# Optimization experiments

Measured on AMD Instinct MI355X. Metric: run time of the kernel, lower is better.

Reference implementation:

```python
import jax, jax.numpy as jnp
import numpy as np

B, N, DIN, DE, NH, DK = 4, 256, 128, 64, 8, 16


def setup_inputs() -> dict:
    key = jax.random.key(0)
    ks = jax.random.split(key, 8)
    s = 0.05
    return {
        "h": jax.random.normal(ks[0], (B, N, DIN), jnp.float32),
        "e": jax.random.normal(ks[1], (B, N, N, DE), jnp.float32),
        "mask": jnp.ones((B, N), jnp.float32),
        "WQ": jax.random.normal(ks[2], (DIN, NH * DK), jnp.float32) * s,
        "WK": jax.random.normal(ks[3], (DIN, NH * DK), jnp.float32) * s,
        "WV": jax.random.normal(ks[4], (DIN, NH * DK), jnp.float32) * s,
        "WE": jax.random.normal(ks[5], (DE, NH * DK), jnp.float32) * s,
        "WE2": jax.random.normal(ks[6], (DE, NH * DK), jnp.float32) * s,
    }


def reference(h, e, mask, WQ, WK, WV, WE, WE2):
    b, n, _ = h.shape
    Q = (h @ WQ).reshape(b, n, NH, DK)
    K = (h @ WK).reshape(b, n, NH, DK) * (float(DK) ** -0.5)
    V = (h @ WV).reshape(b, n, NH, DK)
    E = (e @ WE).reshape(b, n, n, NH, DK)
    E2 = (e @ WE2).reshape(b, n, n, NH, DK)
    # edge-augmented scores: (b, i, j, h, k)
    scores = jnp.einsum('bihk,bjhk->bijh', Q, K)[..., None] + E2
    scores = jnp.exp(jnp.clip(scores, -5.0, 5.0))
    attn_mask = mask[:, :, None, None, None] * mask[:, None, :, None, None]
    scores = scores * attn_mask
    softmax_denom = jnp.clip(scores.sum(axis=2), 1e-6, None)  # (b,i,h,k)
    scores = scores * attn_mask  # attn_dropout p=0.0 -> identity
    out = jnp.einsum('bijhk,bjhk->bihk', scores, V)
    out = out + (scores * E).sum(axis=2)
    out = out / softmax_denom
    return out.reshape(b, n, NH * DK)
```

## Files before the change

### kernel.cpp

```cpp
#include <hip/hip_runtime.h>

#define BB   4
#define NN   256
#define DIN  128
#define DE   64
#define NH   8
#define DK   16
#define CC   128

typedef __attribute__((ext_vector_type(8))) short short8;
typedef __attribute__((ext_vector_type(4))) float f32x4;

__device__ __forceinline__ unsigned short f2bfu(float f) {
    union { float f; unsigned int i; } v; v.f = f;
    unsigned int x = v.i;
    x += 0x7FFFu + ((x >> 16) & 1u);
    return (unsigned short)(x >> 16);
}

__global__ __launch_bounds__(256) void qkv_kernel(
    const float* __restrict__ h, const float* __restrict__ WQ,
    const float* __restrict__ WK, const float* __restrict__ WV,
    const float* __restrict__ WE, const float* __restrict__ WE2,
    float* __restrict__ Qw, float* __restrict__ Kw, float* __restrict__ Vt,
    unsigned short* __restrict__ wfrag)
{
    const int t = threadIdx.x;

    if (blockIdx.x >= 256) {
        const int tid  = (blockIdx.x - 256) * 256 + t;
        const int m    = tid >> 10;
        const int g    = (tid >> 7) & 7;
        const int ks   = (tid >> 6) & 1;
        const int lane = tid & 63;
        const int q4 = lane >> 4, l15 = lane & 15;
        const float* W = m ? WE2 : WE;
        union { uint4 u; unsigned short s[8]; } pk;
        #pragma unroll
        for (int ii = 0; ii < 8; ++ii) {
            const int d = ks * 32 + q4 * 8 + ii;
            pk.s[ii] = f2bfu(W[d * CC + g * 16 + l15]);
        }
        ((uint4*)wfrag)[tid] = pk.u;
        return;
    }

    __shared__ float hsh[4 * DIN];
    __shared__ float psum[4 * 1536];
    const int r0 = blockIdx.x * 4;

    hsh[t]       = h[(size_t)r0 * DIN + t];
    hsh[256 + t] = h[(size_t)r0 * DIN + 256 + t];
    __syncthreads();

    const int cp  = t & 63;
    const int qtr = t >> 6;
    float aq[4][2], ak[4][2], av[4][2];
    #pragma unroll
    for (int r = 0; r < 4; ++r)
        aq[r][0]=aq[r][1]=ak[r][0]=ak[r][1]=av[r][0]=av[r][1]=0.f;

    #pragma unroll 4
    for (int dd = 0; dd < 32; ++dd) {
        const int d = qtr * 32 + dd;
        const float2 fq = ((const float2*)WQ)[d * 64 + cp];
        const float2 fk = ((const float2*)WK)[d * 64 + cp];
        const float2 fv = ((const float2*)WV)[d * 64 + cp];
        #pragma unroll
        for (int r = 0; r < 4; ++r) {
            const float hd = hsh[r * DIN + d];
            aq[r][0] = fmaf(hd, fq.x, aq[r][0]); aq[r][1] = fmaf(hd, fq.y, aq[r][1]);
            ak[r][0] = fmaf(hd, fk.x, ak[r][0]); ak[r][1] = fmaf(hd, fk.y, ak[r][1]);
            av[r][0] = fmaf(hd, fv.x, av[r][0]); av[r][1] = fmaf(hd, fv.y, av[r][1]);
        }
    }
    float* pq = psum + qtr * 1536;
    #pragma unroll
    for (int r = 0; r < 4; ++r) {
        pq[r*384       + 2*cp] = aq[r][0]; pq[r*384       + 2*cp+1] = aq[r][1];
        pq[r*384 + 128 + 2*cp] = ak[r][0]; pq[r*384 + 128 + 2*cp+1] = ak[r][1];
        pq[r*384 + 256 + 2*cp] = av[r][0]; pq[r*384 + 256 + 2*cp+1] = av[r][1];
    }
    __syncthreads();

    const int b  = r0 >> 8;
    const int j0 = r0 & 255;
    #pragma unroll
    for (int k = 0; k < 6; ++k) {
        const int o = k * 256 + t;
        float v = psum[o] + psum[1536 + o] + psum[3072 + o] + psum[4608 + o];
        const int r   = o / 384;
        const int mc  = o - r * 384;
        const int mat = mc >> 7;
        const int c   = mc & 127;
        if      (mat == 0) Qw[(size_t)(r0 + r) * CC + c] = v;
        else if (mat == 1) Kw[(size_t)(r0 + r) * CC + c] = v * 0.25f;
        else               Vt[((size_t)(b * CC) + c) * NN + j0 + r] = v;
    }
}

__global__ __launch_bounds__(256) void attn_kernel(
    const float* __restrict__ e, const float* __restrict__ maskp,
    const unsigned short* __restrict__ wfrag,
    const float* __restrict__ Qw, const float* __restrict__ Kw,
    const float* __restrict__ Vt, float* __restrict__ out)
{
    __shared__ __align__(16) unsigned short esh[128 * DE];
    __shared__ __align__(16) float qk_sh[NH * NN];
    __shared__ __align__(16) float msk_sh[NN];
    __shared__ __align__(16) float qrow_sh[CC];

    const int row  = blockIdx.x;
    const int b    = row >> 8, i = row & 255;
    const int t    = threadIdx.x;
    const int wave = t >> 6, lane = t & 63;
    const int q4   = lane >> 4;
    const int l15  = lane & 15;

    const float4* esrc = (const float4*)(e + (size_t)row * NN * DE);
    uint4* edst = (uint4*)esh;

    short8 bfrag[2][2][2];
    {
        const uint4* wf = (const uint4*)wfrag;
        #pragma unroll
        for (int m = 0; m < 2; ++m)
        #pragma unroll
        for (int ct = 0; ct < 2; ++ct) {
            const int g = wave * 2 + ct;
            #pragma unroll
            for (int ks = 0; ks < 2; ++ks) {
                union { uint4 u; short8 s8; } cv;
                cv.u = wf[((m * 8 + g) * 2 + ks) * 64 + lane];
                bfrag[m][ct][ks] = cv.s8;
            }
        }
    }

    if (t < CC) qrow_sh[t] = Qw[(size_t)row * CC + t];
    msk_sh[t] = maskp[b * NN + t];

    #pragma unroll
    for (int r = 0; r < 4; ++r) {
        const int cidx = r * 256 + t;
        const int j = cidx >> 3, ch = cidx & 7;
        const float4 f0 = esrc[2 * cidx];
        const float4 f1 = esrc[2 * cidx + 1];
        union { uint4 u; unsigned short s[8]; } pk;
        pk.s[0]=f2bfu(f0.x); pk.s[1]=f2bfu(f0.y); pk.s[2]=f2bfu(f0.z); pk.s[3]=f2bfu(f0.w);
        pk.s[4]=f2bfu(f1.x); pk.s[5]=f2bfu(f1.y); pk.s[6]=f2bfu(f1.z); pk.s[7]=f2bfu(f1.w);
        edst[j * 8 + (ch ^ (j & 7))] = pk.u;
    }

    float4 pf[8];
    #pragma unroll
    for (int r = 0; r < 4; ++r) {
        const int cidx = r * 256 + t;
        pf[2*r]     = esrc[2048 + 2 * cidx];
        pf[2*r + 1] = esrc[2048 + 2 * cidx + 1];
    }

    __syncthreads();

    {
        const float4* kr = (const float4*)(Kw + (size_t)(b * NN + t) * CC);
        #pragma unroll
        for (int hh = 0; hh < NH; ++hh) {
            float s = 0.f;
            #pragma unroll
            for (int p = 0; p < 4; ++p) {
                const float4 kv = kr[hh * 4 + p];
                const int qb = hh * 16 + p * 4;
                s += kv.x * qrow_sh[qb]     + kv.y * qrow_sh[qb + 1]
                   + kv.z * qrow_sh[qb + 2] + kv.w * qrow_sh[qb + 3];
            }
            qk_sh[hh * 256 + t] = s;
        }
    }
    __syncthreads();

    const float mi = msk_sh[i];
    float acc[2] = {0.f, 0.f}, dnm[2] = {0.f, 0.f};
    const short8* ep = (const short8*)esh;

    #pragma unroll
    for (int hf = 0; hf < 2; ++hf) {
        if (hf == 1) {
            __syncthreads();
            #pragma unroll
            for (int r = 0; r < 4; ++r) {
                const int cidx = r * 256 + t;
                const int j = cidx >> 3, ch = cidx & 7;
                const float4 f0 = pf[2 * r];
                const float4 f1 = pf[2 * r + 1];
                union { uint4 u; unsigned short s[8]; } pk;
                pk.s[0]=f2bfu(f0.x); pk.s[1]=f2bfu(f0.y); pk.s[2]=f2bfu(f0.z); pk.s[3]=f2bfu(f0.w);
                pk.s[4]=f2bfu(f1.x); pk.s[5]=f2bfu(f1.y); pk.s[6]=f2bfu(f1.z); pk.s[7]=f2bfu(f1.w);
                edst[j * 8 + (ch ^ (j & 7))] = pk.u;
            }
            __syncthreads();
        }
        #pragma unroll 2
        for (int s = 0; s < 8; ++s) {
            const int ja = s * 16 + l15;
            const short8 a0 = ep[ja * 8 + ((q4    ) ^ (ja & 7))];
            const short8 a1 = ep[ja * 8 + ((q4 + 4) ^ (ja & 7))];
            const int j0g = hf * 128 + s * 16 + q4 * 4;
            union { float4 v; float a[4]; } mk4;
            mk4.v = *(const float4*)(msk_sh + j0g);
            #pragma unroll
            for (int ct = 0; ct < 2; ++ct) {
                const int g = wave * 2 + ct;
                f32x4 s2 = {0.f,0.f,0.f,0.f}, eE = {0.f,0.f,0.f,0.f};
                s2 = __builtin_amdgcn_mfma_f32_16x16x32_bf16(a0, bfrag[1][ct][0], s2, 0,0,0);
                s2 = __builtin_amdgcn_mfma_f32_16x16x32_bf16(a1, bfrag[1][ct][1], s2, 0,0,0);
                eE = __builtin_amdgcn_mfma_f32_16x16x32_bf16(a0, bfrag[0][ct][0], eE, 0,0,0);
                eE = __builtin_amdgcn_mfma_f32_16x16x32_bf16(a1, bfrag[0][ct][1], eE, 0,0,0);
                union { float4 v; float a[4]; } v4, qk4;
                v4.v  = *(const float4*)(Vt + ((size_t)(b * CC) + g * 16 + l15) * NN + j0g);
                qk4.v = *(const float4*)(qk_sh + g * 256 + j0g);
                #pragma unroll
                for (int r = 0; r < 4; ++r) {
                    float sc = qk4.a[r] + s2[r];
                    sc = fminf(5.f, fmaxf(-5.f, sc));
                    const float p  = __expf(sc);
                    const float mm = mi * mk4.a[r];
                    const float s1 = p * mm;
                    dnm[ct] += s1;
                    acc[ct] = fmaf(s1 * mm, v4.a[r] + eE[r], acc[ct]);
                }
            }
        }
    }

    #pragma unroll
    for (int ct = 0; ct < 2; ++ct) {
        float a = acc[ct], d = dnm[ct];
        a += __shfl_xor(a, 16); a += __shfl_xor(a, 32);
        d += __shfl_xor(d, 16); d += __shfl_xor(d, 32);
        acc[ct] = a; dnm[ct] = d;
    }
    if (lane < 32) {
        const int ct = lane >> 4;
        out[(size_t)row * CC + wave * 32 + lane] = acc[ct] / fmaxf(dnm[ct], 1e-6f);
    }
}

extern "C" void kernel_launch(void* const* d_in, const int* in_sizes, int n_in,
                              void* d_out, int out_size, void* d_ws, size_t ws_size,
                              hipStream_t stream)
{
    const float* h    = (const float*)d_in[0];
    const float* e    = (const float*)d_in[1];
    const float* mask = (const float*)d_in[2];
    const float* WQ   = (const float*)d_in[3];
    const float* WK   = (const float*)d_in[4];
    const float* WV   = (const float*)d_in[5];
    const float* WE   = (const float*)d_in[6];
    const float* WE2  = (const float*)d_in[7];

    unsigned short* wfrag = (unsigned short*)d_ws;
    float* Qw = (float*)((char*)d_ws + 32768);
    float* Kw = Qw + BB * NN * CC;
    float* Vt = Kw + BB * NN * CC;

    qkv_kernel <<<264,   256, 0, stream>>>(h, WQ, WK, WV, WE, WE2,
                                           Qw, Kw, Vt, wfrag);
    attn_kernel<<<BB*NN, 256, 0, stream>>>(e, mask, wfrag, Qw, Kw, Vt,
                                           (float*)d_out);
}
```

Before: 143.4 us.

## Stage full edge row in LDS, transpose K for coalesced QK loads

K is now written transposed (per batch, channel-major), so each thread's QK dot product reads coalesced columns across threads instead of strided rows. The attention kernel stages all 256 edge rows of bf16 e into a doubled LDS buffer in one pass, removing the two-half prefetch scheme and its extra barriers. Mask and Q-row values are now read straight from global memory instead of being staged in shared memory. The cost is twice the LDS per block, which may reduce occupancy, and the loss of overlap between the second half's e loads and the first half's compute.

```diff
diff --git a/kernel.cpp b/kernel.cpp
--- a/kernel.cpp
+++ b/kernel.cpp
@@ -22,7 +22,7 @@
     const float* __restrict__ h, const float* __restrict__ WQ,
     const float* __restrict__ WK, const float* __restrict__ WV,
     const float* __restrict__ WE, const float* __restrict__ WE2,
-    float* __restrict__ Qw, float* __restrict__ Kw, float* __restrict__ Vt,
+    float* __restrict__ Qw, float* __restrict__ Kt, float* __restrict__ Vt,
     unsigned short* __restrict__ wfrag)
 {
     const int t = threadIdx.x;
@@ -94,7 +94,7 @@
         const int mat = mc >> 7;
         const int c   = mc & 127;
         if      (mat == 0) Qw[(size_t)(r0 + r) * CC + c] = v;
-        else if (mat == 1) Kw[(size_t)(r0 + r) * CC + c] = v * 0.25f;
+        else if (mat == 1) Kt[((size_t)(b * CC) + c) * NN + j0 + r] = v * 0.25f;
         else               Vt[((size_t)(b * CC) + c) * NN + j0 + r] = v;
     }
 }
@@ -102,23 +102,17 @@
 __global__ __launch_bounds__(256) void attn_kernel(
     const float* __restrict__ e, const float* __restrict__ maskp,
     const unsigned short* __restrict__ wfrag,
-    const float* __restrict__ Qw, const float* __restrict__ Kw,
+    const float* __restrict__ Qw, const float* __restrict__ Kt,
     const float* __restrict__ Vt, float* __restrict__ out)
 {
-    __shared__ __align__(16) unsigned short esh[128 * DE];
+    __shared__ __align__(16) unsigned short esh[NN * DE];
     __shared__ __align__(16) float qk_sh[NH * NN];
-    __shared__ __align__(16) float msk_sh[NN];
-    __shared__ __align__(16) float qrow_sh[CC];
 
     const int row  = blockIdx.x;
-    const int b    = row >> 8, i = row & 255;
+    const int b    = row >> 8;
     const int t    = threadIdx.x;
     const int wave = t >> 6, lane = t & 63;
-    const int q4   = lane >> 4;
-    const int l15  = lane & 15;
-
-    const float4* esrc = (const float4*)(e + (size_t)row * NN * DE);
-    uint4* edst = (uint4*)esh;
+    const int q4   = lane >> 4, l15 = lane & 15;
 
     short8 bfrag[2][2][2];
     {
@@ -137,98 +131,68 @@
         }
     }
 
-    if (t < CC) qrow_sh[t] = Qw[(size_t)row * CC + t];
-    msk_sh[t] = maskp[b * NN + t];
-
-    #pragma unroll
-    for (int r = 0; r < 4; ++r) {
-        const int cidx = r * 256 + t;
-        const int j = cidx >> 3, ch = cidx & 7;
-        const float4 f0 = esrc[2 * cidx];
-        const float4 f1 = esrc[2 * cidx + 1];
-        union { uint4 u; unsigned short s[8]; } pk;
-        pk.s[0]=f2bfu(f0.x); pk.s[1]=f2bfu(f0.y); pk.s[2]=f2bfu(f0.z); pk.s[3]=f2bfu(f0.w);
-        pk.s[4]=f2bfu(f1.x); pk.s[5]=f2bfu(f1.y); pk.s[6]=f2bfu(f1.z); pk.s[7]=f2bfu(f1.w);
-        edst[j * 8 + (ch ^ (j & 7))] = pk.u;
-    }
-
-    float4 pf[8];
-    #pragma unroll
-    for (int r = 0; r < 4; ++r) {
-        const int cidx = r * 256 + t;
-        pf[2*r]     = esrc[2048 + 2 * cidx];
-        pf[2*r + 1] = esrc[2048 + 2 * cidx + 1];
-    }
-
-    __syncthreads();
-
     {
-        const float4* kr = (const float4*)(Kw + (size_t)(b * NN + t) * CC);
+        const float4* esrc = (const float4*)(e + (size_t)row * NN * DE);
+        uint4* edst = (uint4*)esh;
+        #pragma unroll
+        for (int r = 0; r < 8; ++r) {
+            const int cidx = r * 256 + t;
+            const int j = cidx >> 3, ch = cidx & 7;
+            const float4 f0 = esrc[2 * cidx];
+            const float4 f1 = esrc[2 * cidx + 1];
+            union { uint4 u; unsigned short s[8]; } pk;
+            pk.s[0]=f2bfu(f0.x); pk.s[1]=f2bfu(f0.y); pk.s[2]=f2bfu(f0.z); pk.s[3]=f2bfu(f0.w);
+            pk.s[4]=f2bfu(f1.x); pk.s[5]=f2bfu(f1.y); pk.s[6]=f2bfu(f1.z); pk.s[7]=f2bfu(f1.w);
+            edst[j * 8 + (ch ^ (j & 7))] = pk.u;
+        }
+    }
+
+    {
+        const float* qp = Qw + (size_t)row * CC;
+        const float* kp = Kt + (size_t)(b * CC) * NN + t;
         #pragma unroll
         for (int hh = 0; hh < NH; ++hh) {
             float s = 0.f;
             #pragma unroll
-            for (int p = 0; p < 4; ++p) {
-                const float4 kv = kr[hh * 4 + p];
-                const int qb = hh * 16 + p * 4;
-                s += kv.x * qrow_sh[qb]     + kv.y * qrow_sh[qb + 1]
-                   + kv.z * qrow_sh[qb + 2] + kv.w * qrow_sh[qb + 3];
-            }
-            qk_sh[hh * 256 + t] = s;
+            for (int kk = 0; kk < DK; ++kk)
+                s = fmaf(qp[hh * DK + kk], kp[(size_t)(hh * DK + kk) * NN], s);
+            qk_sh[hh * NN + t] = s;
         }
     }
     __syncthreads();
 
-    const float mi = msk_sh[i];
+    const float mi = maskp[row];
     float acc[2] = {0.f, 0.f}, dnm[2] = {0.f, 0.f};
     const short8* ep = (const short8*)esh;
 
-    #pragma unroll
-    for (int hf = 0; hf < 2; ++hf) {
-        if (hf == 1) {
-            __syncthreads();
+    #pragma unroll 4
+    for (int s = 0; s < 16; ++s) {
+        const int ja = s * 16 + l15;
+        const short8 a0 = ep[ja * 8 + ((q4    ) ^ (ja & 7))];
+        const short8 a1 = ep[ja * 8 + ((q4 + 4) ^ (ja & 7))];
+        const int j0 = s * 16 + q4 * 4;
+        union { float4 v; float a[4]; } mk4;
+        mk4.v = *(const float4*)(maskp + b * NN + j0);
+        #pragma unroll
+        for (int ct = 0; ct < 2; ++ct) {
+            const int g = wave * 2 + ct;
+            f32x4 s2 = {0.f,0.f,0.f,0.f}, eE = {0.f,0.f,0.f,0.f};
+            s2 = __builtin_amdgcn_mfma_f32_16x16x32_bf16(a0, bfrag[1][ct][0], s2, 0,0,0);
+            s2 = __builtin_amdgcn_mfma_f32_16x16x32_bf16(a1, bfrag[1][ct][1], s2, 0,0,0);
+            eE = __builtin_amdgcn_mfma_f32_16x16x32_bf16(a0, bfrag[0][ct][0], eE, 0,0,0);
+            eE = __builtin_amdgcn_mfma_f32_16x16x32_bf16(a1, bfrag[0][ct][1], eE, 0,0,0);
+            union { float4 v; float a[4]; } v4, qk4;
+            v4.v  = *(const float4*)(Vt + ((size_t)(b * CC) + g * 16 + l15) * NN + j0);
+            qk4.v = *(const float4*)(qk_sh + g * NN + j0);
             #pragma unroll
             for (int r = 0; r < 4; ++r) {
-                const int cidx = r * 256 + t;
-                const int j = cidx >> 3, ch = cidx & 7;
-                const float4 f0 = pf[2 * r];
-                const float4 f1 = pf[2 * r + 1];
-                union { uint4 u; unsigned short s[8]; } pk;
-                pk.s[0]=f2bfu(f0.x); pk.s[1]=f2bfu(f0.y); pk.s[2]=f2bfu(f0.z); pk.s[3]=f2bfu(f0.w);
-                pk.s[4]=f2bfu(f1.x); pk.s[5]=f2bfu(f1.y); pk.s[6]=f2bfu(f1.z); pk.s[7]=f2bfu(f1.w);
-                edst[j * 8 + (ch ^ (j & 7))] = pk.u;
-            }
-            __syncthreads();
-        }
-        #pragma unroll 2
-        for (int s = 0; s < 8; ++s) {
-            const int ja = s * 16 + l15;
-            const short8 a0 = ep[ja * 8 + ((q4    ) ^ (ja & 7))];
-            const short8 a1 = ep[ja * 8 + ((q4 + 4) ^ (ja & 7))];
-            const int j0g = hf * 128 + s * 16 + q4 * 4;
-            union { float4 v; float a[4]; } mk4;
-            mk4.v = *(const float4*)(msk_sh + j0g);
-            #pragma unroll
-            for (int ct = 0; ct < 2; ++ct) {
-                const int g = wave * 2 + ct;
-                f32x4 s2 = {0.f,0.f,0.f,0.f}, eE = {0.f,0.f,0.f,0.f};
-                s2 = __builtin_amdgcn_mfma_f32_16x16x32_bf16(a0, bfrag[1][ct][0], s2, 0,0,0);
-                s2 = __builtin_amdgcn_mfma_f32_16x16x32_bf16(a1, bfrag[1][ct][1], s2, 0,0,0);
-                eE = __builtin_amdgcn_mfma_f32_16x16x32_bf16(a0, bfrag[0][ct][0], eE, 0,0,0);
-                eE = __builtin_amdgcn_mfma_f32_16x16x32_bf16(a1, bfrag[0][ct][1], eE, 0,0,0);
-                union { float4 v; float a[4]; } v4, qk4;
-                v4.v  = *(const float4*)(Vt + ((size_t)(b * CC) + g * 16 + l15) * NN + j0g);
-                qk4.v = *(const float4*)(qk_sh + g * 256 + j0g);
-                #pragma unroll
-                for (int r = 0; r < 4; ++r) {
-                    float sc = qk4.a[r] + s2[r];
-                    sc = fminf(5.f, fmaxf(-5.f, sc));
-                    const float p  = __expf(sc);
-                    const float mm = mi * mk4.a[r];
-                    const float s1 = p * mm;
-                    dnm[ct] += s1;
-                    acc[ct] = fmaf(s1 * mm, v4.a[r] + eE[r], acc[ct]);
-                }
+                float sc = qk4.a[r] + s2[r];
+                sc = fminf(5.f, fmaxf(-5.f, sc));
+                const float p  = __expf(sc);
+                const float mm = mi * mk4.a[r];
+                const float s1 = p * mm;
+                dnm[ct] += s1;
+                acc[ct] = fmaf(s1 * mm, v4.a[r] + eE[r], acc[ct]);
             }
         }
     }
@@ -261,11 +225,11 @@
 
     unsigned short* wfrag = (unsigned short*)d_ws;
     float* Qw = (float*)((char*)d_ws + 32768);
-    float* Kw = Qw + BB * NN * CC;
-    float* Vt = Kw + BB * NN * CC;
+    float* Kt = Qw + BB * NN * CC;
+    float* Vt = Kt + BB * NN * CC;
 
     qkv_kernel <<<264,   256, 0, stream>>>(h, WQ, WK, WV, WE, WE2,
-                                           Qw, Kw, Vt, wfrag);
-    attn_kernel<<<BB*NN, 256, 0, stream>>>(e, mask, wfrag, Qw, Kw, Vt,
+                                           Qw, Kt, Vt, wfrag);
+    attn_kernel<<<BB*NN, 256, 0, stream>>>(e, mask, wfrag, Qw, Kt, Vt,
                                            (float*)d_out);
 }
```

Result: faster. 140.5 us (-2.1%).
